# Performance work log

Hardware: AMD Instinct MI355X
Metric: run time of the kernel (lower is better)

Reference implementation:

```python
import jax, jax.numpy as jnp
import numpy as np

TEMPERATURE = 64.0
AUGMENT_K = 16
EPS = 1e-8

def _l2norm(x, axis=-1):
    n = jnp.sqrt(jnp.sum(x * x, axis=axis, keepdims=True))
    return x / jnp.maximum(n, EPS)

def setup_inputs() -> dict:
    key = jax.random.key(0)
    k1, k2, k3 = jax.random.split(key, 3)
    support = jax.random.normal(k1, (1, 5, 5, 640), dtype=jnp.float32)   # [B, shot, way, d]
    query = jax.random.normal(k2, (1, 15, 5, 640), dtype=jnp.float32)    # [B, nq, way, d]
    memory = jax.random.normal(k3, (300000, 640), dtype=jnp.float32)     # memory bank [M, d]
    return {"support": support, "query": query, "memory": memory}

def reference(support, query, memory):
    B, n_shot, n_way, d = support.shape
    M = memory.shape[0]
    # basic prototype = mean over shots, L2-normalized (get_similarity_scores)
    basic_proto = _l2norm(support.mean(axis=1))                 # [B, way, d]
    # cosine similarity of support entries and memory entries vs basic proto.
    # Avoid materializing shot_memory expanded to [B, shot+M, way, d]:
    sim_sup = jnp.einsum('bswd,bwd->bsw', _l2norm(support), basic_proto)   # [B, shot, way]
    sim_mem = jnp.einsum('md,bwd->bmw', _l2norm(memory), basic_proto)      # [B, M, way]
    # mask weights: 1.0 for support slots, 0.2 for memory slots
    sim = jnp.concatenate([sim_sup, 0.2 * sim_mem], axis=1)                # [B, shot+M, way]
    # top-k over the (shot+M) axis, per way
    sim_t = jnp.transpose(sim, (0, 2, 1))                                  # [B, way, shot+M]
    sim_topk, ind = jax.lax.top_k(sim_t, AUGMENT_K)                        # [B, way, K]
    # gather embeddings: index < shot -> support, else memory[index - shot]
    is_sup = ind < n_shot
    sup_idx = jnp.clip(ind, 0, n_shot - 1)
    mem_idx = jnp.clip(ind - n_shot, 0, M - 1)
    sup_wsd = jnp.transpose(support, (0, 2, 1, 3))                         # [B, way, shot, d]
    sup_g = jnp.take_along_axis(sup_wsd, sup_idx[..., None], axis=2)       # [B, way, K, d]
    mem_g = memory[mem_idx]                                                # [B, way, K, d]
    shot_topk = jnp.where(is_sup[..., None], sup_g, mem_g)                 # [B, way, K, d]
    # similarity-weighted prototype
    proto = jnp.sum(sim_topk[..., None] * shot_topk, axis=2) / jnp.sum(sim_topk, axis=2)[..., None]  # [B, way, d]
    # cosine-similarity logits (proto normalized, query NOT normalized, per original)
    proto_n = _l2norm(proto)
    q = query.reshape(B, -1, d)                                            # [B, nq*way, d]
    logits = jnp.einsum('bqd,bpd->bqp', q, proto_n) / TEMPERATURE
    return logits.reshape(-1, n_way)                                       # [nq*way, way]
```

## Files before the change

kernel.cpp:

```cpp
#include <hip/hip_runtime.h>
#include <float.h>

#define WAY   5
#define SHOT  5
#define DIM   640
#define KTOP  16
#define EPSN  1e-8f

#define B_BLOCKS  1024
#define B_THREADS 256
#define WPB       (B_THREADS / 64)
#define B_WAVES   (B_BLOCKS * WPB)
#define RPI       8
#define ROWSTRIDE (B_WAVES * RPI)

#define SEGS   32
#define CANDS  (SEGS * KTOP)

#define OFF_PROTO   0
#define OFF_SIMSUP  (WAY * DIM)
#define OFF_PROTOW  (OFF_SIMSUP + 32)
#define OFF_CANDV   (OFF_PROTOW + WAY * DIM)
#define OFF_CANDI   (OFF_CANDV + WAY * CANDS)
#define OFF_SIM     (OFF_CANDI + WAY * CANDS)

__device__ __forceinline__ float blockReduce256(float v, float* sred) {
#pragma unroll
  for (int off = 32; off >= 1; off >>= 1) v += __shfl_xor(v, off, 64);
  __syncthreads();
  if ((threadIdx.x & 63) == 0) sred[threadIdx.x >> 6] = v;
  __syncthreads();
  return sred[0] + sred[1] + sred[2] + sred[3];
}

template <int CTRL>
__device__ __forceinline__ float dppMov(float x) {
  int r = __builtin_amdgcn_update_dpp(0, __builtin_bit_cast(int, x), CTRL, 0xF, 0xF, true);
  return __builtin_bit_cast(float, r);
}
__device__ __forceinline__ float rowReduce16(float v) {
  v += dppMov<0x128>(v);
  v += dppMov<0x124>(v);
  v += dppMov<0x122>(v);
  v += dppMov<0x121>(v);
  return v;
}

__global__ __launch_bounds__(256) void protoA_kernel(
    const float* __restrict__ support, float* __restrict__ ws) {
  const int w = blockIdx.x;
  const int tid = threadIdx.x;
  __shared__ float sred[4];

  float m[3];
  float n2 = 0.f;
#pragma unroll
  for (int c = 0; c < 3; ++c) {
    const int t = tid + 256 * c;
    float v = 0.f;
    if (t < DIM) {
#pragma unroll
      for (int s = 0; s < SHOT; ++s) v += support[(s * WAY + w) * DIM + t];
      v *= (1.0f / SHOT);
    }
    m[c] = v;
    n2 += v * v;
  }
  n2 = blockReduce256(n2, sred);
  const float inv = 1.0f / fmaxf(sqrtf(n2), EPSN);

#pragma unroll
  for (int c = 0; c < 3; ++c) {
    const int t = tid + 256 * c;
    if (t < DIM) ws[OFF_PROTO + w * DIM + t] = m[c] * inv;
  }

  for (int s = 0; s < SHOT; ++s) {
    float dot = 0.f, sn2 = 0.f;
#pragma unroll
    for (int c = 0; c < 3; ++c) {
      const int t = tid + 256 * c;
      if (t < DIM) {
        const float sv = support[(s * WAY + w) * DIM + t];
        dot += sv * (m[c] * inv);
        sn2 += sv * sv;
      }
    }
    dot = blockReduce256(dot, sred);
    sn2 = blockReduce256(sn2, sred);
    if (tid == 0)
      ws[OFF_SIMSUP + s * WAY + w] = dot / fmaxf(sqrtf(sn2), EPSN);
  }
}

__global__ __launch_bounds__(B_THREADS) void simB1_kernel(
    const float* __restrict__ memory, const float* __restrict__ ws,
    float* __restrict__ simAll, int M) {
  __shared__ float sP[WAY * DIM];
  for (int i = threadIdx.x; i < WAY * DIM / 4; i += B_THREADS)
    ((float4*)sP)[i] = ((const float4*)(ws + OFF_PROTO))[i];
  __syncthreads();

  const int lane = threadIdx.x & 63;
  const int sub  = lane & 15;
  const int grp  = lane >> 4;
  const int waveId = blockIdx.x * WPB + (threadIdx.x >> 6);
  const int colOff = sub * 4;
  const float* sPc = sP + colOff;

  for (int base = waveId * RPI; base < M; base += ROWSTRIDE) {
    const int rA = base + grp;
    const int rB = base + 4 + grp;
    const bool okA = (rA < M);
    const bool okB = (rB < M);
    const size_t offA = (size_t)(okA ? rA : (M - 1)) * DIM + colOff;
    const size_t offB = (size_t)(okB ? rB : (M - 1)) * DIM + colOff;

    float nA = 0.f, a0 = 0.f, a1 = 0.f, a2 = 0.f, a3 = 0.f, a4 = 0.f;
    float nB = 0.f, b0 = 0.f, b1 = 0.f, b2 = 0.f, b3 = 0.f, b4 = 0.f;
#pragma unroll
    for (int it = 0; it < 10; ++it) {
      const float4 xa = *(const float4*)&memory[offA + it * 64];
      const float4 xb = *(const float4*)&memory[offB + it * 64];
      const float4 p0 = *(const float4*)&sPc[0 * DIM + it * 64];
      const float4 p1 = *(const float4*)&sPc[1 * DIM + it * 64];
      const float4 p2 = *(const float4*)&sPc[2 * DIM + it * 64];
      const float4 p3 = *(const float4*)&sPc[3 * DIM + it * 64];
      const float4 p4 = *(const float4*)&sPc[4 * DIM + it * 64];
      nA = fmaf(xa.x, xa.x, fmaf(xa.y, xa.y, fmaf(xa.z, xa.z, fmaf(xa.w, xa.w, nA))));
      a0 = fmaf(xa.x, p0.x, fmaf(xa.y, p0.y, fmaf(xa.z, p0.z, fmaf(xa.w, p0.w, a0))));
      a1 = fmaf(xa.x, p1.x, fmaf(xa.y, p1.y, fmaf(xa.z, p1.z, fmaf(xa.w, p1.w, a1))));
      a2 = fmaf(xa.x, p2.x, fmaf(xa.y, p2.y, fmaf(xa.z, p2.z, fmaf(xa.w, p2.w, a2))));
      a3 = fmaf(xa.x, p3.x, fmaf(xa.y, p3.y, fmaf(xa.z, p3.z, fmaf(xa.w, p3.w, a3))));
      a4 = fmaf(xa.x, p4.x, fmaf(xa.y, p4.y, fmaf(xa.z, p4.z, fmaf(xa.w, p4.w, a4))));
      nB = fmaf(xb.x, xb.x, fmaf(xb.y, xb.y, fmaf(xb.z, xb.z, fmaf(xb.w, xb.w, nB))));
      b0 = fmaf(xb.x, p0.x, fmaf(xb.y, p0.y, fmaf(xb.z, p0.z, fmaf(xb.w, p0.w, b0))));
      b1 = fmaf(xb.x, p1.x, fmaf(xb.y, p1.y, fmaf(xb.z, p1.z, fmaf(xb.w, p1.w, b1))));
      b2 = fmaf(xb.x, p2.x, fmaf(xb.y, p2.y, fmaf(xb.z, p2.z, fmaf(xb.w, p2.w, b2))));
      b3 = fmaf(xb.x, p3.x, fmaf(xb.y, p3.y, fmaf(xb.z, p3.z, fmaf(xb.w, p3.w, b3))));
      b4 = fmaf(xb.x, p4.x, fmaf(xb.y, p4.y, fmaf(xb.z, p4.z, fmaf(xb.w, p4.w, b4))));
    }

    const float rA0 = rowReduce16(a0), rA1 = rowReduce16(a1), rA2 = rowReduce16(a2);
    const float rA3 = rowReduce16(a3), rA4 = rowReduce16(a4), rAn = rowReduce16(nA);
    const float rB0 = rowReduce16(b0), rB1 = rowReduce16(b1), rB2 = rowReduce16(b2);
    const float rB3 = rowReduce16(b3), rB4 = rowReduce16(b4), rBn = rowReduce16(nB);

    const float sA = 0.2f / fmaxf(sqrtf(rAn), EPSN);
    const float sB = 0.2f / fmaxf(sqrtf(rBn), EPSN);
    float vA = rA0, vB = rB0;
    vA = (sub == 1) ? rA1 : vA;  vB = (sub == 1) ? rB1 : vB;
    vA = (sub == 2) ? rA2 : vA;  vB = (sub == 2) ? rB2 : vB;
    vA = (sub == 3) ? rA3 : vA;  vB = (sub == 3) ? rB3 : vB;
    vA = (sub == 4) ? rA4 : vA;  vB = (sub == 4) ? rB4 : vB;
    if (okA && sub < WAY) simAll[(size_t)sub * M + rA] = vA * sA;
    if (okB && sub < WAY) simAll[(size_t)sub * M + rB] = vB * sB;
  }
}

__global__ __launch_bounds__(256) void topkC1_kernel(
    const float* __restrict__ simAll, float* __restrict__ candV,
    int* __restrict__ candI, int M) {
  const int w   = blockIdx.x / SEGS;
  const int seg = blockIdx.x % SEGS;
  const int tid = threadIdx.x;
  const int len = (M + SEGS - 1) / SEGS;
  const int i0 = seg * len;
  const int i1 = min(i0 + len, M);

  float lv[KTOP];
  int   li[KTOP];
#pragma unroll
  for (int k = 0; k < KTOP; ++k) { lv[k] = -FLT_MAX; li[k] = 0; }

  const float* sv = simAll + (size_t)w * M;
  for (int i = i0 + tid; i < i1; i += 256) {
    const float v = sv[i];
    if (v > lv[KTOP - 1]) {
      const int id = SHOT + i;
#pragma unroll
      for (int j = KTOP - 1; j >= 1; --j) {
        const float up = lv[j - 1];
        const int   ui = li[j - 1];
        const bool shift = (up < v);
        const float cur = lv[j];
        const int  curi = li[j];
        lv[j] = shift ? up : (cur < v ? v : cur);
        li[j] = shift ? ui : (cur < v ? id : curi);
      }
      if (lv[0] < v) { li[0] = id; lv[0] = v; }
    }
  }

  __shared__ float sLV[256][KTOP];
  __shared__ int   sLI[256][KTOP];
  __shared__ float sWv[4];
  __shared__ int   sWi[4];
#pragma unroll
  for (int k = 0; k < KTOP; ++k) { sLV[tid][k] = lv[k]; sLI[tid][k] = li[k]; }
  __syncthreads();

  int cursor = 0;
  for (int r = 0; r < KTOP; ++r) {
    float v = (cursor < KTOP) ? sLV[tid][cursor] : -FLT_MAX;
    int   t = tid;
#pragma unroll
    for (int off = 32; off >= 1; off >>= 1) {
      const float ov = __shfl_xor(v, off, 64);
      const int   ot = __shfl_xor(t, off, 64);
      if (ov > v) { v = ov; t = ot; }
    }
    __syncthreads();
    if ((tid & 63) == 0) { sWv[tid >> 6] = v; sWi[tid >> 6] = t; }
    __syncthreads();
    float bv = sWv[0]; int bt = sWi[0];
#pragma unroll
    for (int q = 1; q < 4; ++q)
      if (sWv[q] > bv) { bv = sWv[q]; bt = sWi[q]; }
    if (tid == bt) {
      candV[(size_t)(w * SEGS + seg) * KTOP + r] = sLV[tid][cursor];
      candI[(size_t)(w * SEGS + seg) * KTOP + r] = sLI[tid][cursor];
      ++cursor;
    }
    __syncthreads();
  }
}

__global__ __launch_bounds__(256) void topkProtoC2_kernel(
    const float* __restrict__ support, const float* __restrict__ memory,
    float* __restrict__ ws, const float* __restrict__ candV,
    const int* __restrict__ candI, int M) {
  const int w = blockIdx.x;
  const int tid = threadIdx.x;

  float lv[KTOP];
  int   li[KTOP];
#pragma unroll
  for (int k = 0; k < KTOP; ++k) { lv[k] = -FLT_MAX; li[k] = 0; }
  if (tid < SHOT) {
    lv[0] = ws[OFF_SIMSUP + tid * WAY + w];
    li[0] = tid;
  }

  const float* cv = candV + (size_t)w * CANDS;
  const int*   ci = candI + (size_t)w * CANDS;
  for (int i = tid; i < CANDS; i += 256) {
    const float v = cv[i];
    if (v > lv[KTOP - 1]) {
      const int id = ci[i];
#pragma unroll
      for (int j = KTOP - 1; j >= 1; --j) {
        const float up = lv[j - 1];
        const int   ui = li[j - 1];
        const bool shift = (up < v);
        const float cur = lv[j];
        const int  curi = li[j];
        lv[j] = shift ? up : (cur < v ? v : cur);
        li[j] = shift ? ui : (cur < v ? id : curi);
      }
      if (lv[0] < v) { li[0] = id; lv[0] = v; }
    }
  }

  __shared__ float sLV[256][KTOP];
  __shared__ int   sLI[256][KTOP];
  __shared__ float outV[KTOP];
  __shared__ int   outI[KTOP];
  __shared__ float sWv[4];
  __shared__ int   sWi[4];
  __shared__ float sred[4];
#pragma unroll
  for (int k = 0; k < KTOP; ++k) { sLV[tid][k] = lv[k]; sLI[tid][k] = li[k]; }
  __syncthreads();

  int cursor = 0;
  for (int r = 0; r < KTOP; ++r) {
    float v = (cursor < KTOP) ? sLV[tid][cursor] : -FLT_MAX;
    int   t = tid;
#pragma unroll
    for (int off = 32; off >= 1; off >>= 1) {
      const float ov = __shfl_xor(v, off, 64);
      const int   ot = __shfl_xor(t, off, 64);
      if (ov > v) { v = ov; t = ot; }
    }
    __syncthreads();
    if ((tid & 63) == 0) { sWv[tid >> 6] = v; sWi[tid >> 6] = t; }
    __syncthreads();
    float bv = sWv[0]; int bt = sWi[0];
#pragma unroll
    for (int q = 1; q < 4; ++q)
      if (sWv[q] > bv) { bv = sWv[q]; bt = sWi[q]; }
    if (tid == bt) {
      outV[r] = sLV[tid][cursor];
      outI[r] = sLI[tid][cursor];
      ++cursor;
    }
    __syncthreads();
  }

  float sumW = 0.f;
#pragma unroll
  for (int k = 0; k < KTOP; ++k) sumW += outV[k];

  float pw[3];
  float n2 = 0.f;
#pragma unroll
  for (int c = 0; c < 3; ++c) {
    const int t = tid + 256 * c;
    float acc = 0.f;
    if (t < DIM) {
#pragma unroll
      for (int k = 0; k < KTOP; ++k) {
        const int gi = outI[k];
        const float* emb = (gi < SHOT)
            ? (support + (size_t)(gi * WAY + w) * DIM)
            : (memory + (size_t)(gi - SHOT) * DIM);
        acc += outV[k] * emb[t];
      }
      acc /= sumW;
    }
    pw[c] = acc;
    n2 += acc * acc;
  }
  n2 = blockReduce256(n2, sred);
  const float inv = 1.0f / fmaxf(sqrtf(n2), EPSN);
#pragma unroll
  for (int c = 0; c < 3; ++c) {
    const int t = tid + 256 * c;
    if (t < DIM) ws[OFF_PROTOW + w * DIM + t] = pw[c] * inv;
  }
}

__global__ __launch_bounds__(64) void logitsD_kernel(
    const float* __restrict__ query, const float* __restrict__ ws,
    float* __restrict__ out) {
  const int q = blockIdx.x;
  const int p = blockIdx.y;
  const int lane = threadIdx.x;
  const float* qr = query + (size_t)q * DIM;
  const float* pn = ws + OFF_PROTOW + p * DIM;
  float acc = 0.f;
#pragma unroll
  for (int k = 0; k < 5; ++k) {
    const float2 a = *(const float2*)&qr[2 * (lane + 64 * k)];
    const float2 b = *(const float2*)&pn[2 * (lane + 64 * k)];
    acc += a.x * b.x + a.y * b.y;
  }
#pragma unroll
  for (int off = 32; off >= 1; off >>= 1) acc += __shfl_xor(acc, off, 64);
  if (lane == 0) out[q * WAY + p] = acc * (1.0f / 64.0f);
}

extern "C" void kernel_launch(void* const* d_in, const int* in_sizes, int n_in,
                              void* d_out, int out_size, void* d_ws, size_t ws_size,
                              hipStream_t stream) {
  const float* support = (const float*)d_in[0];
  const float* query   = (const float*)d_in[1];
  const float* memory  = (const float*)d_in[2];
  float* out = (float*)d_out;
  float* ws  = (float*)d_ws;
  const int M = in_sizes[2] / DIM;

  float* candV  = ws + OFF_CANDV;
  int*   candI  = (int*)(ws + OFF_CANDI);
  float* simAll = ws + OFF_SIM;

  hipLaunchKernelGGL(protoA_kernel, dim3(WAY), dim3(256), 0, stream, support, ws);
  hipLaunchKernelGGL(simB1_kernel, dim3(B_BLOCKS), dim3(B_THREADS), 0, stream,
                     memory, ws, simAll, M);
  hipLaunchKernelGGL(topkC1_kernel, dim3(WAY * SEGS), dim3(256), 0, stream,
                     simAll, candV, candI, M);
  hipLaunchKernelGGL(topkProtoC2_kernel, dim3(WAY), dim3(256), 0, stream,
                     support, memory, ws, candV, candI, M);
  hipLaunchKernelGGL(logitsD_kernel, dim3(75, WAY), dim3(64), 0, stream,
                     query, ws, out);
}
```

Before: 198.9 us.

## Fuse prototype build into similarity kernel and use nontemporal memory loads

Removes the separate protoA launch: each block of the similarity kernel now recomputes the normalized mean prototypes from support straight into LDS, and the support-similarity scores are computed inside the top-k/proto kernel. Memory-bank reads switch to nontemporal loads so the 768MB stream does not pollute cache. This saves one kernel launch and a dependency. In exchange, every one of the 1024 blocks redundantly reads the support tensor and runs serial block reductions before starting its main loop.

```diff
diff --git a/kernel.cpp b/kernel.cpp
--- a/kernel.cpp
+++ b/kernel.cpp
@@ -17,12 +17,7 @@
 #define SEGS   32
 #define CANDS  (SEGS * KTOP)
 
-#define OFF_PROTO   0
-#define OFF_SIMSUP  (WAY * DIM)
-#define OFF_PROTOW  (OFF_SIMSUP + 32)
-#define OFF_CANDV   (OFF_PROTOW + WAY * DIM)
-#define OFF_CANDI   (OFF_CANDV + WAY * CANDS)
-#define OFF_SIM     (OFF_CANDI + WAY * CANDS)
+typedef float floatx4 __attribute__((ext_vector_type(4)));
 
 __device__ __forceinline__ float blockReduce256(float v, float* sred) {
 #pragma unroll
@@ -46,60 +41,41 @@
   return v;
 }
 
-__global__ __launch_bounds__(256) void protoA_kernel(
-    const float* __restrict__ support, float* __restrict__ ws) {
-  const int w = blockIdx.x;
+__device__ __forceinline__ void buildProtosLDS(
+    const float* __restrict__ support, float* sP, float* sred) {
   const int tid = threadIdx.x;
-  __shared__ float sred[4];
-
-  float m[3];
-  float n2 = 0.f;
-#pragma unroll
-  for (int c = 0; c < 3; ++c) {
-    const int t = tid + 256 * c;
+  for (int idx = tid; idx < WAY * DIM; idx += B_THREADS) {
+    const int w = idx / DIM, t = idx - w * DIM;
     float v = 0.f;
-    if (t < DIM) {
-#pragma unroll
-      for (int s = 0; s < SHOT; ++s) v += support[(s * WAY + w) * DIM + t];
-      v *= (1.0f / SHOT);
-    }
-    m[c] = v;
-    n2 += v * v;
-  }
-  n2 = blockReduce256(n2, sred);
-  const float inv = 1.0f / fmaxf(sqrtf(n2), EPSN);
-
-#pragma unroll
-  for (int c = 0; c < 3; ++c) {
-    const int t = tid + 256 * c;
-    if (t < DIM) ws[OFF_PROTO + w * DIM + t] = m[c] * inv;
-  }
-
-  for (int s = 0; s < SHOT; ++s) {
-    float dot = 0.f, sn2 = 0.f;
+#pragma unroll
+    for (int s = 0; s < SHOT; ++s) v += support[(s * WAY + w) * DIM + t];
+    sP[w * DIM + t] = v * (1.0f / SHOT);
+  }
+  __syncthreads();
+  for (int w = 0; w < WAY; ++w) {
+    float n2 = 0.f;
 #pragma unroll
     for (int c = 0; c < 3; ++c) {
       const int t = tid + 256 * c;
-      if (t < DIM) {
-        const float sv = support[(s * WAY + w) * DIM + t];
-        dot += sv * (m[c] * inv);
-        sn2 += sv * sv;
-      }
-    }
-    dot = blockReduce256(dot, sred);
-    sn2 = blockReduce256(sn2, sred);
-    if (tid == 0)
-      ws[OFF_SIMSUP + s * WAY + w] = dot / fmaxf(sqrtf(sn2), EPSN);
-  }
-}
-
-__global__ __launch_bounds__(B_THREADS) void simB1_kernel(
-    const float* __restrict__ memory, const float* __restrict__ ws,
+      if (t < DIM) { const float m = sP[w * DIM + t]; n2 = fmaf(m, m, n2); }
+    }
+    n2 = blockReduce256(n2, sred);
+    const float inv = 1.0f / fmaxf(sqrtf(n2), EPSN);
+#pragma unroll
+    for (int c = 0; c < 3; ++c) {
+      const int t = tid + 256 * c;
+      if (t < DIM) sP[w * DIM + t] *= inv;
+    }
+  }
+  __syncthreads();
+}
+
+__global__ __launch_bounds__(B_THREADS) void simB1f_kernel(
+    const float* __restrict__ support, const float* __restrict__ memory,
     float* __restrict__ simAll, int M) {
   __shared__ float sP[WAY * DIM];
-  for (int i = threadIdx.x; i < WAY * DIM / 4; i += B_THREADS)
-    ((float4*)sP)[i] = ((const float4*)(ws + OFF_PROTO))[i];
-  __syncthreads();
+  __shared__ float sred[4];
+  buildProtosLDS(support, sP, sred);
 
   const int lane = threadIdx.x & 63;
   const int sub  = lane & 15;
@@ -120,8 +96,8 @@
     float nB = 0.f, b0 = 0.f, b1 = 0.f, b2 = 0.f, b3 = 0.f, b4 = 0.f;
 #pragma unroll
     for (int it = 0; it < 10; ++it) {
-      const float4 xa = *(const float4*)&memory[offA + it * 64];
-      const float4 xb = *(const float4*)&memory[offB + it * 64];
+      const floatx4 xa = __builtin_nontemporal_load((const floatx4*)&memory[offA + it * 64]);
+      const floatx4 xb = __builtin_nontemporal_load((const floatx4*)&memory[offB + it * 64]);
       const float4 p0 = *(const float4*)&sPc[0 * DIM + it * 64];
       const float4 p1 = *(const float4*)&sPc[1 * DIM + it * 64];
       const float4 p2 = *(const float4*)&sPc[2 * DIM + it * 64];
@@ -228,19 +204,52 @@
 
 __global__ __launch_bounds__(256) void topkProtoC2_kernel(
     const float* __restrict__ support, const float* __restrict__ memory,
-    float* __restrict__ ws, const float* __restrict__ candV,
-    const int* __restrict__ candI, int M) {
+    const float* __restrict__ candV, const int* __restrict__ candI,
+    float* __restrict__ protoW, int M) {
   const int w = blockIdx.x;
   const int tid = threadIdx.x;
+  __shared__ float simsup[SHOT];
+  __shared__ float sred[4];
+
+  float m[3];
+  float n2 = 0.f;
+#pragma unroll
+  for (int c = 0; c < 3; ++c) {
+    const int t = tid + 256 * c;
+    float v = 0.f;
+    if (t < DIM) {
+#pragma unroll
+      for (int s = 0; s < SHOT; ++s) v += support[(s * WAY + w) * DIM + t];
+      v *= (1.0f / SHOT);
+    }
+    m[c] = v;
+    n2 += v * v;
+  }
+  n2 = blockReduce256(n2, sred);
+  const float inv0 = 1.0f / fmaxf(sqrtf(n2), EPSN);
+
+  for (int s = 0; s < SHOT; ++s) {
+    float dot = 0.f, sn2 = 0.f;
+#pragma unroll
+    for (int c = 0; c < 3; ++c) {
+      const int t = tid + 256 * c;
+      if (t < DIM) {
+        const float sv = support[(s * WAY + w) * DIM + t];
+        dot += sv * (m[c] * inv0);
+        sn2 += sv * sv;
+      }
+    }
+    dot = blockReduce256(dot, sred);
+    sn2 = blockReduce256(sn2, sred);
+    if (tid == 0) simsup[s] = dot / fmaxf(sqrtf(sn2), EPSN);
+  }
+  __syncthreads();
 
   float lv[KTOP];
   int   li[KTOP];
 #pragma unroll
   for (int k = 0; k < KTOP; ++k) { lv[k] = -FLT_MAX; li[k] = 0; }
-  if (tid < SHOT) {
-    lv[0] = ws[OFF_SIMSUP + tid * WAY + w];
-    li[0] = tid;
-  }
+  if (tid < SHOT) { lv[0] = simsup[tid]; li[0] = tid; }
 
   const float* cv = candV + (size_t)w * CANDS;
   const int*   ci = candI + (size_t)w * CANDS;
@@ -268,7 +277,6 @@
   __shared__ int   outI[KTOP];
   __shared__ float sWv[4];
   __shared__ int   sWi[4];
-  __shared__ float sred[4];
 #pragma unroll
   for (int k = 0; k < KTOP; ++k) { sLV[tid][k] = lv[k]; sLI[tid][k] = li[k]; }
   __syncthreads();
@@ -303,7 +311,7 @@
   for (int k = 0; k < KTOP; ++k) sumW += outV[k];
 
   float pw[3];
-  float n2 = 0.f;
+  float pn2 = 0.f;
 #pragma unroll
   for (int c = 0; c < 3; ++c) {
     const int t = tid + 256 * c;
@@ -320,25 +328,25 @@
       acc /= sumW;
     }
     pw[c] = acc;
-    n2 += acc * acc;
-  }
-  n2 = blockReduce256(n2, sred);
-  const float inv = 1.0f / fmaxf(sqrtf(n2), EPSN);
+    pn2 += acc * acc;
+  }
+  pn2 = blockReduce256(pn2, sred);
+  const float inv1 = 1.0f / fmaxf(sqrtf(pn2), EPSN);
 #pragma unroll
   for (int c = 0; c < 3; ++c) {
     const int t = tid + 256 * c;
-    if (t < DIM) ws[OFF_PROTOW + w * DIM + t] = pw[c] * inv;
+    if (t < DIM) protoW[w * DIM + t] = pw[c] * inv1;
   }
 }
 
 __global__ __launch_bounds__(64) void logitsD_kernel(
-    const float* __restrict__ query, const float* __restrict__ ws,
+    const float* __restrict__ query, const float* __restrict__ protoW,
     float* __restrict__ out) {
   const int q = blockIdx.x;
   const int p = blockIdx.y;
   const int lane = threadIdx.x;
   const float* qr = query + (size_t)q * DIM;
-  const float* pn = ws + OFF_PROTOW + p * DIM;
+  const float* pn = protoW + p * DIM;
   float acc = 0.f;
 #pragma unroll
   for (int k = 0; k < 5; ++k) {
@@ -361,17 +369,17 @@
   float* ws  = (float*)d_ws;
   const int M = in_sizes[2] / DIM;
 
-  float* candV  = ws + OFF_CANDV;
-  int*   candI  = (int*)(ws + OFF_CANDI);
-  float* simAll = ws + OFF_SIM;
-
-  hipLaunchKernelGGL(protoA_kernel, dim3(WAY), dim3(256), 0, stream, support, ws);
-  hipLaunchKernelGGL(simB1_kernel, dim3(B_BLOCKS), dim3(B_THREADS), 0, stream,
-                     memory, ws, simAll, M);
+  float* simAll = ws;
+  float* candV  = ws + (size_t)WAY * M;
+  int*   candI  = (int*)(candV + WAY * CANDS);
+  float* protoW = (float*)(candI + WAY * CANDS);
+
+  hipLaunchKernelGGL(simB1f_kernel, dim3(B_BLOCKS), dim3(B_THREADS), 0, stream,
+                     support, memory, simAll, M);
   hipLaunchKernelGGL(topkC1_kernel, dim3(WAY * SEGS), dim3(256), 0, stream,
                      simAll, candV, candI, M);
   hipLaunchKernelGGL(topkProtoC2_kernel, dim3(WAY), dim3(256), 0, stream,
-                     support, memory, ws, candV, candI, M);
+                     support, memory, candV, candI, protoW, M);
   hipLaunchKernelGGL(logitsD_kernel, dim3(75, WAY), dim3(64), 0, stream,
-                     query, ws, out);
-}
+                     query, protoW, out);
+}
```

Result: faster. 183.3 us (-7.9%).
